# Kernel tuning notes

Measured on AMD Instinct MI355X. Metric: run time of the kernel, lower is better.

## Reference

```python
import jax, jax.numpy as jnp
import numpy as np

NUM_HEADS = 12
FEATURE_DIM = 16
HEAD_DIM = 128
EPS = 1e-12


def taylor_map(x):
    # x: [b, h, t, d] -> [b, h, t, 1 + d + d*d] (2nd-order Taylor features of exp)
    d = x.shape[-1]
    r2 = jnp.asarray(np.sqrt(2.0), x.dtype)
    rd = jnp.asarray(np.sqrt(d), x.dtype)
    rrd = jnp.asarray(np.sqrt(np.sqrt(d)), x.dtype)
    x2 = (x[..., :, None] * x[..., None, :]).reshape(x.shape[:-1] + (d * d,)) / r2
    ones = jnp.ones(x.shape[:-1] + (1,), x.dtype)
    return jnp.concatenate([ones, x / rrd, x2 / rd], axis=-1)


def setup_inputs() -> dict:
    key = jax.random.key(0)
    ks = jax.random.split(key, 5)
    b, t, hid = 2, 2048, 1536
    scale = 0.02
    return {
        "hidden_states": jax.random.normal(ks[0], (b, t, hid), jnp.float32),
        "Wq": jax.random.normal(ks[1], (NUM_HEADS * FEATURE_DIM, hid), jnp.float32) * scale,
        "Wk": jax.random.normal(ks[2], (NUM_HEADS * FEATURE_DIM, hid), jnp.float32) * scale,
        "Wv": jax.random.normal(ks[3], (NUM_HEADS * HEAD_DIM, hid), jnp.float32) * scale,
        "Wo": jax.random.normal(ks[4], (hid, NUM_HEADS * HEAD_DIM), jnp.float32) * scale,
    }


def reference(hidden_states, Wq, Wk, Wv, Wo):
    b, t, _ = hidden_states.shape
    H, dk, dv = NUM_HEADS, FEATURE_DIM, HEAD_DIM
    # projections (torch Linear: x @ W^T), split heads -> [b, h, t, d]
    q = (hidden_states @ Wq.T).reshape(b, t, H, dk).transpose(0, 2, 1, 3)
    k = (hidden_states @ Wk.T).reshape(b, t, H, dk).transpose(0, 2, 1, 3)
    v = (hidden_states @ Wv.T).reshape(b, t, H, dv).transpose(0, 2, 1, 3)
    qf = taylor_map(q)  # [b, h, t, D], D = 1 + dk + dk^2
    kf = taylor_map(k)
    # causal kernelized attention: identical math to cumsum-of-outer-products form
    S = jnp.einsum("bhtd,bhsd->bhts", qf, kf)  # [b, h, t, t]
    mask = jnp.tril(jnp.ones((t, t), bool))
    S = jnp.where(mask, S, jnp.zeros((), S.dtype))
    num = jnp.einsum("bhts,bhse->bhte", S, v)  # [b, h, t, dv]
    den = S.sum(-1) + EPS  # [b, h, t]
    y = num / den[..., None]
    y = y.transpose(0, 2, 1, 3).reshape(b, t, H * dv)
    return y @ Wo.T
```

## Files before the change

### kernel.cpp

```cpp
#include <hip/hip_runtime.h>

#define B 2
#define T 2048
#define HID 1536
#define NH 12
#define DK 16
#define DV 128
#define BT (B * T)
#define EPS 1e-12f

typedef __attribute__((ext_vector_type(8))) short bf16x8;
typedef __attribute__((ext_vector_type(4))) float f32x4;

__device__ int g_taskctr;

__device__ __forceinline__ unsigned short f2bf(float f) {
    unsigned int u = __float_as_uint(f);
    u += 0x7FFFu + ((u >> 16) & 1u);
    return (unsigned short)(u >> 16);
}

__device__ __forceinline__ unsigned int cvt_pk_bf16(float lo, float hi) {
    unsigned int r;
    asm("v_cvt_pk_bf16_f32 %0, %1, %2" : "=v"(r) : "v"(lo), "v"(hi));
    return r;
}

__global__ __launch_bounds__(256) void cvt_all(const float* __restrict__ hs,
                                               const float* __restrict__ Wq,
                                               const float* __restrict__ Wk,
                                               const float* __restrict__ Wv,
                                               const float* __restrict__ Wo,
                                               unsigned short* __restrict__ hsb,
                                               unsigned short* __restrict__ wqk,
                                               unsigned short* __restrict__ wvb,
                                               unsigned short* __restrict__ wob) {
    int bx = blockIdx.x;
    if (bx == 0 && threadIdx.x == 0) g_taskctr = 512;
    const float* src;
    unsigned short* dst;
    if (bx < 3072)      { src = hs; dst = hsb; }
    else if (bx < 3216) { src = Wq; dst = wqk;          bx -= 3072; }
    else if (bx < 3360) { src = Wk; dst = wqk + 294912; bx -= 3216; }
    else if (bx < 4512) { src = Wv; dst = wvb;          bx -= 3360; }
    else                { src = Wo; dst = wob;          bx -= 4512; }
    const int i = (bx * 256 + threadIdx.x) * 8;
    float4 a = *(const float4*)(src + i);
    float4 b = *(const float4*)(src + i + 4);
    *(ushort4*)(dst + i)     = make_ushort4(f2bf(a.x), f2bf(a.y), f2bf(a.z), f2bf(a.w));
    *(ushort4*)(dst + i + 4) = make_ushort4(f2bf(b.x), f2bf(b.y), f2bf(b.z), f2bf(b.w));
}

__device__ __forceinline__ void gemm_tile_bf16(const unsigned short* __restrict__ A,
                                               const unsigned short* __restrict__ Bm,
                                               unsigned short* __restrict__ C,
                                               int m0, int n0, int K, int ldc,
                                               unsigned short* As, unsigned short* Bs) {
    const int tid = threadIdx.x;
    const int wave = tid >> 6, lane = tid & 63;
    const int wm = (wave & 1) * 64, wn = (wave >> 1) * 64;
    const int fr = lane & 15;
    const int fk = (lane >> 4) * 8;

    f32x4 acc[4][4];
#pragma unroll
    for (int i = 0; i < 4; ++i)
#pragma unroll
        for (int j = 0; j < 4; ++j) acc[i][j] = (f32x4)0.f;

    const int c0 = tid, c1 = tid + 256;
    const int r0 = c0 >> 2, q0 = (c0 & 3) * 8;
    const int r1 = c1 >> 2, q1 = (c1 & 3) * 8;

    for (int k0 = 0; k0 < K; k0 += 32) {
        __builtin_amdgcn_global_load_lds(
            (const __attribute__((address_space(1))) void*)(A + (size_t)(m0 + r0) * K + k0 + q0),
            (__attribute__((address_space(3))) void*)(As + c0 * 8), 16, 0, 0);
        __builtin_amdgcn_global_load_lds(
            (const __attribute__((address_space(1))) void*)(A + (size_t)(m0 + r1) * K + k0 + q1),
            (__attribute__((address_space(3))) void*)(As + c1 * 8), 16, 0, 0);
        __builtin_amdgcn_global_load_lds(
            (const __attribute__((address_space(1))) void*)(Bm + (size_t)(n0 + r0) * K + k0 + q0),
            (__attribute__((address_space(3))) void*)(Bs + c0 * 8), 16, 0, 0);
        __builtin_amdgcn_global_load_lds(
            (const __attribute__((address_space(1))) void*)(Bm + (size_t)(n0 + r1) * K + k0 + q1),
            (__attribute__((address_space(3))) void*)(Bs + c1 * 8), 16, 0, 0);
        __syncthreads();

        bf16x8 af[4], bfr[4];
#pragma unroll
        for (int mb = 0; mb < 4; ++mb)
            af[mb] = *(const bf16x8*)(As + (wm + mb * 16 + fr) * 32 + fk);
#pragma unroll
        for (int nb = 0; nb < 4; ++nb)
            bfr[nb] = *(const bf16x8*)(Bs + (wn + nb * 16 + fr) * 32 + fk);
#pragma unroll
        for (int mb = 0; mb < 4; ++mb)
#pragma unroll
            for (int nb = 0; nb < 4; ++nb)
                acc[mb][nb] = __builtin_amdgcn_mfma_f32_16x16x32_bf16(
                    af[mb], bfr[nb], acc[mb][nb], 0, 0, 0);
        __syncthreads();
    }

    const int orow = (lane >> 4) * 4;
#pragma unroll
    for (int nb = 0; nb < 4; ++nb) {
        const int col = n0 + wn + nb * 16 + fr;
#pragma unroll
        for (int mb = 0; mb < 4; ++mb) {
            const int row = m0 + wm + mb * 16 + orow;
#pragma unroll
            for (int r = 0; r < 4; ++r)
                C[(size_t)(row + r) * ldc + col] = f2bf(acc[mb][nb][r]);
        }
    }
}

__global__ __launch_bounds__(256) void proj_qkv(const unsigned short* __restrict__ hsb,
                                                const unsigned short* __restrict__ wqk,
                                                const unsigned short* __restrict__ wvb,
                                                unsigned short* __restrict__ qkb,
                                                unsigned short* __restrict__ vtg) {
    __shared__ unsigned short As[128 * 32];
    __shared__ unsigned short Bs[128 * 32];
    const int bx = blockIdx.x;
    if (bx < 96) {
        gemm_tile_bf16(hsb, wqk, qkb, (bx / 3) * 128, (bx % 3) * 128, HID, 384, As, Bs);
    } else {
        const int vid = bx - 96;
        const int grp = vid / 48, sub = vid % 48;
        const int n_t = grp * 4 + (sub & 3), m_t = sub >> 2;
        gemm_tile_bf16(wvb, hsb, vtg, m_t * 128, n_t * 128, HID, BT, As, Bs);
    }
}

__global__ __launch_bounds__(256) void proj_out(const unsigned short* __restrict__ A,
                                                const unsigned short* __restrict__ Bm,
                                                float* __restrict__ C) {
    __shared__ unsigned short As[128 * 32];
    __shared__ unsigned short Bs[128 * 32];
    const int tid = threadIdx.x;
    const int m0 = blockIdx.y * 128;
    const int n0 = blockIdx.x * 128;
    const int wave = tid >> 6, lane = tid & 63;
    const int wm = (wave & 1) * 64, wn = (wave >> 1) * 64;
    const int fr = lane & 15;
    const int fk = (lane >> 4) * 8;
    const int K = HID;

    f32x4 acc[4][4];
#pragma unroll
    for (int i = 0; i < 4; ++i)
#pragma unroll
        for (int j = 0; j < 4; ++j) acc[i][j] = (f32x4)0.f;

    const int c0 = tid, c1 = tid + 256;
    const int r0 = c0 >> 2, q0 = (c0 & 3) * 8;
    const int r1 = c1 >> 2, q1 = (c1 & 3) * 8;

    for (int k0 = 0; k0 < K; k0 += 32) {
        __builtin_amdgcn_global_load_lds(
            (const __attribute__((address_space(1))) void*)(A + (size_t)(m0 + r0) * K + k0 + q0),
            (__attribute__((address_space(3))) void*)(As + c0 * 8), 16, 0, 0);
        __builtin_amdgcn_global_load_lds(
            (const __attribute__((address_space(1))) void*)(A + (size_t)(m0 + r1) * K + k0 + q1),
            (__attribute__((address_space(3))) void*)(As + c1 * 8), 16, 0, 0);
        __builtin_amdgcn_global_load_lds(
            (const __attribute__((address_space(1))) void*)(Bm + (size_t)(n0 + r0) * K + k0 + q0),
            (__attribute__((address_space(3))) void*)(Bs + c0 * 8), 16, 0, 0);
        __builtin_amdgcn_global_load_lds(
            (const __attribute__((address_space(1))) void*)(Bm + (size_t)(n0 + r1) * K + k0 + q1),
            (__attribute__((address_space(3))) void*)(Bs + c1 * 8), 16, 0, 0);
        __syncthreads();

        bf16x8 af[4], bfr[4];
#pragma unroll
        for (int mb = 0; mb < 4; ++mb)
            af[mb] = *(const bf16x8*)(As + (wm + mb * 16 + fr) * 32 + fk);
#pragma unroll
        for (int nb = 0; nb < 4; ++nb)
            bfr[nb] = *(const bf16x8*)(Bs + (wn + nb * 16 + fr) * 32 + fk);
#pragma unroll
        for (int mb = 0; mb < 4; ++mb)
#pragma unroll
            for (int nb = 0; nb < 4; ++nb)
                acc[mb][nb] = __builtin_amdgcn_mfma_f32_16x16x32_bf16(
                    af[mb], bfr[nb], acc[mb][nb], 0, 0, 0);
        __syncthreads();
    }

    const int orow = (lane >> 4) * 4;
#pragma unroll
    for (int nb = 0; nb < 4; ++nb) {
        const int col = n0 + wn + nb * 16 + fr;
#pragma unroll
        for (int mb = 0; mb < 4; ++mb) {
            const int row = m0 + wm + mb * 16 + orow;
#pragma unroll
            for (int r = 0; r < 4; ++r)
                C[(size_t)(row + r) * HID + col] = acc[mb][nb][r];
        }
    }
}

__global__ __launch_bounds__(256) void based_attn_mfma(const unsigned short* __restrict__ qk,
                                                       const unsigned short* __restrict__ vt,
                                                       unsigned short* __restrict__ yb) {
    const int tid = threadIdx.x;
    const int wave = tid >> 6, lane = tid & 63;
    const int fr = lane & 15, quad = lane >> 4;
    const int fk = quad * 8;
    const int fkk = (quad & 1) * 8;

    __shared__ __attribute__((aligned(16))) unsigned short ss[2][64][72];
    __shared__ float den_lds[64];
    __shared__ int task_s;

    int c = blockIdx.x;

    for (;;) {
        if (c >= 768) break;
        const int r = (c < 512) ? ((c & 1) ? 767 - (c >> 1) : (c >> 1)) : (c - 256);
        const int qt = 31 - r / 24;
        const int hb = r % 24;
        const int h  = hb >> 1;
        const int bi = hb & 1;

        if (tid < 64) den_lds[tid] = 0.f;

        const bf16x8 zf = {};
        bf16x8 qf[4];
#pragma unroll
        for (int nt = 0; nt < 4; ++nt) {
            qf[nt] = zf;
            if (quad < 2)
                qf[nt] = *(const bf16x8*)&qk[(size_t)(bi * T + qt * 64 + nt * 16 + fr) * 384
                                             + h * DK + fk];
        }

        f32x4 oacc[2][4];
#pragma unroll
        for (int mt = 0; mt < 2; ++mt)
#pragma unroll
            for (int nt = 0; nt < 4; ++nt) oacc[mt][nt] = (f32x4)0.f;
        float denp[4] = {0.f, 0.f, 0.f, 0.f};

        const unsigned short* kbase = qk + (size_t)(bi * T + wave * 16 + fr) * 384
                                      + 192 + h * DK + fkk;
        const unsigned short* vbase0 = vt + (size_t)(h * DV + wave * 32 + fr) * BT + bi * T + fk;
        const unsigned short* vbase1 = vbase0 + (size_t)16 * BT;

        bf16x8 kf_n = *(const bf16x8*)kbase;
        bf16x8 vf_n[2][2];
        vf_n[0][0] = *(const bf16x8*)(vbase0);
        vf_n[0][1] = *(const bf16x8*)(vbase0 + 32);
        vf_n[1][0] = *(const bf16x8*)(vbase1);
        vf_n[1][1] = *(const bf16x8*)(vbase1 + 32);

        for (int kt = 0; kt <= qt; ++kt) {
            const int bsel = kt & 1;
            const bf16x8 kf = kf_n;
            bf16x8 vf[2][2];
            vf[0][0] = vf_n[0][0]; vf[0][1] = vf_n[0][1];
            vf[1][0] = vf_n[1][0]; vf[1][1] = vf_n[1][1];

            {
                const int ktn = (kt < qt) ? kt + 1 : qt;
                kf_n = *(const bf16x8*)(kbase + (size_t)ktn * 64 * 384);
                const int off = ktn * 64;
                vf_n[0][0] = *(const bf16x8*)(vbase0 + off);
                vf_n[0][1] = *(const bf16x8*)(vbase0 + off + 32);
                vf_n[1][0] = *(const bf16x8*)(vbase1 + off);
                vf_n[1][1] = *(const bf16x8*)(vbase1 + off + 32);
            }

            f32x4 sa[4];
#pragma unroll
            for (int nt = 0; nt < 4; ++nt)
                sa[nt] = __builtin_amdgcn_mfma_f32_16x16x32_bf16(kf, qf[nt], (f32x4)0.f, 0, 0, 0);

#pragma unroll
            for (int nt = 0; nt < 4; ++nt) {
                const int i = nt * 16 + fr;
                float sv[4];
#pragma unroll
                for (int rr = 0; rr < 4; ++rr) {
                    const float a = sa[nt][rr];
                    sv[rr] = fmaf(a, fmaf(a, 1.f / 32.f, 0.25f), 1.f);
                }
                if (kt == qt) {
#pragma unroll
                    for (int rr = 0; rr < 4; ++rr) {
                        const int j = wave * 16 + quad * 4 + rr;
                        if (j > i) sv[rr] = 0.f;
                    }
                }
                denp[nt] += (sv[0] + sv[1]) + (sv[2] + sv[3]);
                uint2 pk;
                pk.x = cvt_pk_bf16(sv[0], sv[1]);
                pk.y = cvt_pk_bf16(sv[2], sv[3]);
                *(uint2*)&ss[bsel][i][wave * 16 + quad * 4] = pk;
            }
            __syncthreads();

#pragma unroll
            for (int k2 = 0; k2 < 2; ++k2) {
                bf16x8 sf[4];
#pragma unroll
                for (int nt = 0; nt < 4; ++nt)
                    sf[nt] = *(const bf16x8*)&ss[bsel][nt * 16 + fr][k2 * 32 + fk];
#pragma unroll
                for (int mt = 0; mt < 2; ++mt)
#pragma unroll
                    for (int nt = 0; nt < 4; ++nt)
                        oacc[mt][nt] = __builtin_amdgcn_mfma_f32_16x16x32_bf16(
                            vf[mt][k2], sf[nt], oacc[mt][nt], 0, 0, 0);
            }
        }

#pragma unroll
        for (int nt = 0; nt < 4; ++nt) {
            float v = denp[nt];
            v += __shfl_xor(v, 16);
            v += __shfl_xor(v, 32);
            if (quad == 0) atomicAdd(&den_lds[nt * 16 + fr], v);
        }
        __syncthreads();

#pragma unroll
        for (int nt = 0; nt < 4; ++nt) {
            const int i = nt * 16 + fr;
            const float rd = 1.f / (den_lds[i] + EPS);
            const size_t rowbase = (size_t)(bi * T + qt * 64 + i) * (NH * DV) + h * DV;
#pragma unroll
            for (int mt = 0; mt < 2; ++mt) {
                const int cc = wave * 32 + mt * 16 + quad * 4;
                const f32x4 o = oacc[mt][nt];
                *(ushort4*)&yb[rowbase + cc] = make_ushort4(f2bf(o[0] * rd), f2bf(o[1] * rd),
                                                            f2bf(o[2] * rd), f2bf(o[3] * rd));
            }
        }

        __syncthreads();
        if (tid == 0) task_s = atomicAdd(&g_taskctr, 1);
        __syncthreads();
        c = task_s;
    }
}

extern "C" void kernel_launch(void* const* d_in, const int* in_sizes, int n_in,
                              void* d_out, int out_size, void* d_ws, size_t ws_size,
                              hipStream_t stream) {
    (void)in_sizes; (void)n_in; (void)out_size; (void)ws_size;
    const float* hs = (const float*)d_in[0];
    const float* Wq = (const float*)d_in[1];
    const float* Wk = (const float*)d_in[2];
    const float* Wv = (const float*)d_in[3];
    const float* Wo = (const float*)d_in[4];
    float* out = (float*)d_out;

    unsigned short* hsb = (unsigned short*)d_ws;
    unsigned short* wqk = hsb + (size_t)BT * HID;
    unsigned short* wvb = wqk + (size_t)384 * HID;
    unsigned short* wob = wvb + (size_t)HID * HID;
    unsigned short* qkb = wob + (size_t)HID * HID;
    unsigned short* vtg = qkb + (size_t)BT * 384;
    unsigned short* ybb = vtg + (size_t)HID * BT;

    dim3 blk(256);
    cvt_all<<<dim3(5664), blk, 0, stream>>>(hs, Wq, Wk, Wv, Wo, hsb, wqk, wvb, wob);

    proj_qkv<<<dim3(480), blk, 0, stream>>>(hsb, wqk, wvb, qkb, vtg);

    based_attn_mfma<<<dim3(512), blk, 0, stream>>>(qkb, vtg, ybb);

    proj_out<<<dim3(12, 32), blk, 0, stream>>>(ybb, wob, out);
}
```

Before: 209.7 us.

## Fuse all four kernels into one persistent kernel with grid barriers

Replaces the four separate launches (conversion, QKV projection, attention, output projection) with a single persistent kernel of 512 blocks that runs each stage in turn, separated by a software grid-wide barrier built on global atomics. The aim is to remove the launch gaps and tail idle time between kernels. The cost is spin-wait barriers and fewer blocks for the conversion stage, which now loops over its work. The barrier also relies on all 512 blocks being resident at once (launch_bounds 256,2), or it can deadlock.

```diff
diff --git a/kernel.cpp b/kernel.cpp
--- a/kernel.cpp
+++ b/kernel.cpp
@@ -13,6 +13,8 @@
 typedef __attribute__((ext_vector_type(4))) float f32x4;
 
 __device__ int g_taskctr;
+__device__ unsigned g_bar_cnt = 0;
+__device__ unsigned g_bar_gen = 0;
 
 __device__ __forceinline__ unsigned short f2bf(float f) {
     unsigned int u = __float_as_uint(f);
@@ -26,29 +28,27 @@
     return r;
 }
 
-__global__ __launch_bounds__(256) void cvt_all(const float* __restrict__ hs,
-                                               const float* __restrict__ Wq,
-                                               const float* __restrict__ Wk,
-                                               const float* __restrict__ Wv,
-                                               const float* __restrict__ Wo,
-                                               unsigned short* __restrict__ hsb,
-                                               unsigned short* __restrict__ wqk,
-                                               unsigned short* __restrict__ wvb,
-                                               unsigned short* __restrict__ wob) {
-    int bx = blockIdx.x;
-    if (bx == 0 && threadIdx.x == 0) g_taskctr = 512;
-    const float* src;
-    unsigned short* dst;
-    if (bx < 3072)      { src = hs; dst = hsb; }
-    else if (bx < 3216) { src = Wq; dst = wqk;          bx -= 3072; }
-    else if (bx < 3360) { src = Wk; dst = wqk + 294912; bx -= 3216; }
-    else if (bx < 4512) { src = Wv; dst = wvb;          bx -= 3360; }
-    else                { src = Wo; dst = wob;          bx -= 4512; }
-    const int i = (bx * 256 + threadIdx.x) * 8;
-    float4 a = *(const float4*)(src + i);
-    float4 b = *(const float4*)(src + i + 4);
-    *(ushort4*)(dst + i)     = make_ushort4(f2bf(a.x), f2bf(a.y), f2bf(a.z), f2bf(a.w));
-    *(ushort4*)(dst + i + 4) = make_ushort4(f2bf(b.x), f2bf(b.y), f2bf(b.z), f2bf(b.w));
+__device__ __forceinline__ void grid_barrier() {
+    __syncthreads();
+    if (threadIdx.x == 0) {
+        __threadfence();
+        unsigned gen = __hip_atomic_load(&g_bar_gen, __ATOMIC_RELAXED,
+                                         __HIP_MEMORY_SCOPE_AGENT);
+        unsigned n = __hip_atomic_fetch_add(&g_bar_cnt, 1u, __ATOMIC_ACQ_REL,
+                                            __HIP_MEMORY_SCOPE_AGENT);
+        if (n + 1u == gridDim.x) {
+            __hip_atomic_store(&g_bar_cnt, 0u, __ATOMIC_RELAXED,
+                               __HIP_MEMORY_SCOPE_AGENT);
+            __hip_atomic_store(&g_bar_gen, gen + 1u, __ATOMIC_RELEASE,
+                               __HIP_MEMORY_SCOPE_AGENT);
+        } else {
+            while (__hip_atomic_load(&g_bar_gen, __ATOMIC_ACQUIRE,
+                                     __HIP_MEMORY_SCOPE_AGENT) == gen)
+                __builtin_amdgcn_s_sleep(1);
+        }
+        __threadfence();
+    }
+    __syncthreads();
 }
 
 __device__ __forceinline__ void gemm_tile_bf16(const unsigned short* __restrict__ A,
@@ -117,37 +117,16 @@
     }
 }
 
-__global__ __launch_bounds__(256) void proj_qkv(const unsigned short* __restrict__ hsb,
-                                                const unsigned short* __restrict__ wqk,
-                                                const unsigned short* __restrict__ wvb,
-                                                unsigned short* __restrict__ qkb,
-                                                unsigned short* __restrict__ vtg) {
-    __shared__ unsigned short As[128 * 32];
-    __shared__ unsigned short Bs[128 * 32];
-    const int bx = blockIdx.x;
-    if (bx < 96) {
-        gemm_tile_bf16(hsb, wqk, qkb, (bx / 3) * 128, (bx % 3) * 128, HID, 384, As, Bs);
-    } else {
-        const int vid = bx - 96;
-        const int grp = vid / 48, sub = vid % 48;
-        const int n_t = grp * 4 + (sub & 3), m_t = sub >> 2;
-        gemm_tile_bf16(wvb, hsb, vtg, m_t * 128, n_t * 128, HID, BT, As, Bs);
-    }
-}
-
-__global__ __launch_bounds__(256) void proj_out(const unsigned short* __restrict__ A,
-                                                const unsigned short* __restrict__ Bm,
-                                                float* __restrict__ C) {
-    __shared__ unsigned short As[128 * 32];
-    __shared__ unsigned short Bs[128 * 32];
+__device__ __forceinline__ void gemm_tile_f32(const unsigned short* __restrict__ A,
+                                              const unsigned short* __restrict__ Bm,
+                                              float* __restrict__ C,
+                                              int m0, int n0, int K, int ldc,
+                                              unsigned short* As, unsigned short* Bs) {
     const int tid = threadIdx.x;
-    const int m0 = blockIdx.y * 128;
-    const int n0 = blockIdx.x * 128;
     const int wave = tid >> 6, lane = tid & 63;
     const int wm = (wave & 1) * 64, wn = (wave >> 1) * 64;
     const int fr = lane & 15;
     const int fk = (lane >> 4) * 8;
-    const int K = HID;
 
     f32x4 acc[4][4];
 #pragma unroll
@@ -199,153 +178,211 @@
             const int row = m0 + wm + mb * 16 + orow;
 #pragma unroll
             for (int r = 0; r < 4; ++r)
-                C[(size_t)(row + r) * HID + col] = acc[mb][nb][r];
-        }
-    }
-}
-
-__global__ __launch_bounds__(256) void based_attn_mfma(const unsigned short* __restrict__ qk,
-                                                       const unsigned short* __restrict__ vt,
-                                                       unsigned short* __restrict__ yb) {
+                C[(size_t)(row + r) * ldc + col] = acc[mb][nb][r];
+        }
+    }
+}
+
+__global__ __launch_bounds__(256, 2) void fused_all(const float* __restrict__ hs,
+                                                    const float* __restrict__ Wq,
+                                                    const float* __restrict__ Wk,
+                                                    const float* __restrict__ Wv,
+                                                    const float* __restrict__ Wo,
+                                                    unsigned short* __restrict__ hsb,
+                                                    unsigned short* __restrict__ wqk,
+                                                    unsigned short* __restrict__ wvb,
+                                                    unsigned short* __restrict__ wob,
+                                                    unsigned short* __restrict__ qkb,
+                                                    unsigned short* __restrict__ vtg,
+                                                    unsigned short* __restrict__ ybb,
+                                                    float* __restrict__ out) {
+    __shared__ __attribute__((aligned(16))) unsigned short smem[9348];
+    const int bid = blockIdx.x;
     const int tid = threadIdx.x;
-    const int wave = tid >> 6, lane = tid & 63;
-    const int fr = lane & 15, quad = lane >> 4;
-    const int fk = quad * 8;
-    const int fkk = (quad & 1) * 8;
-
-    __shared__ __attribute__((aligned(16))) unsigned short ss[2][64][72];
-    __shared__ float den_lds[64];
-    __shared__ int task_s;
-
-    int c = blockIdx.x;
-
-    for (;;) {
-        if (c >= 768) break;
-        const int r = (c < 512) ? ((c & 1) ? 767 - (c >> 1) : (c >> 1)) : (c - 256);
-        const int qt = 31 - r / 24;
-        const int hb = r % 24;
-        const int h  = hb >> 1;
-        const int bi = hb & 1;
-
-        if (tid < 64) den_lds[tid] = 0.f;
-
-        const bf16x8 zf = {};
-        bf16x8 qf[4];
-#pragma unroll
-        for (int nt = 0; nt < 4; ++nt) {
-            qf[nt] = zf;
-            if (quad < 2)
-                qf[nt] = *(const bf16x8*)&qk[(size_t)(bi * T + qt * 64 + nt * 16 + fr) * 384
-                                             + h * DK + fk];
-        }
-
-        f32x4 oacc[2][4];
-#pragma unroll
-        for (int mt = 0; mt < 2; ++mt)
-#pragma unroll
-            for (int nt = 0; nt < 4; ++nt) oacc[mt][nt] = (f32x4)0.f;
-        float denp[4] = {0.f, 0.f, 0.f, 0.f};
-
-        const unsigned short* kbase = qk + (size_t)(bi * T + wave * 16 + fr) * 384
-                                      + 192 + h * DK + fkk;
-        const unsigned short* vbase0 = vt + (size_t)(h * DV + wave * 32 + fr) * BT + bi * T + fk;
-        const unsigned short* vbase1 = vbase0 + (size_t)16 * BT;
-
-        bf16x8 kf_n = *(const bf16x8*)kbase;
-        bf16x8 vf_n[2][2];
-        vf_n[0][0] = *(const bf16x8*)(vbase0);
-        vf_n[0][1] = *(const bf16x8*)(vbase0 + 32);
-        vf_n[1][0] = *(const bf16x8*)(vbase1);
-        vf_n[1][1] = *(const bf16x8*)(vbase1 + 32);
-
-        for (int kt = 0; kt <= qt; ++kt) {
-            const int bsel = kt & 1;
-            const bf16x8 kf = kf_n;
-            bf16x8 vf[2][2];
-            vf[0][0] = vf_n[0][0]; vf[0][1] = vf_n[0][1];
-            vf[1][0] = vf_n[1][0]; vf[1][1] = vf_n[1][1];
-
-            {
-                const int ktn = (kt < qt) ? kt + 1 : qt;
-                kf_n = *(const bf16x8*)(kbase + (size_t)ktn * 64 * 384);
-                const int off = ktn * 64;
-                vf_n[0][0] = *(const bf16x8*)(vbase0 + off);
-                vf_n[0][1] = *(const bf16x8*)(vbase0 + off + 32);
-                vf_n[1][0] = *(const bf16x8*)(vbase1 + off);
-                vf_n[1][1] = *(const bf16x8*)(vbase1 + off + 32);
+
+    if (bid == 0 && tid == 0) g_taskctr = 512;
+    for (int u = bid; u < 5664; u += 512) {
+        int bx = u;
+        const float* src;
+        unsigned short* dst;
+        if (bx < 3072)      { src = hs; dst = hsb; }
+        else if (bx < 3216) { src = Wq; dst = wqk;          bx -= 3072; }
+        else if (bx < 3360) { src = Wk; dst = wqk + 294912; bx -= 3216; }
+        else if (bx < 4512) { src = Wv; dst = wvb;          bx -= 3360; }
+        else                { src = Wo; dst = wob;          bx -= 4512; }
+        const int i = (bx * 256 + tid) * 8;
+        float4 a = *(const float4*)(src + i);
+        float4 b = *(const float4*)(src + i + 4);
+        *(ushort4*)(dst + i)     = make_ushort4(f2bf(a.x), f2bf(a.y), f2bf(a.z), f2bf(a.w));
+        *(ushort4*)(dst + i + 4) = make_ushort4(f2bf(b.x), f2bf(b.y), f2bf(b.z), f2bf(b.w));
+    }
+    grid_barrier();
+
+    {
+        unsigned short* As = smem;
+        unsigned short* Bs = smem + 4096;
+        if (bid < 96) {
+            gemm_tile_bf16(hsb, wqk, qkb, (bid / 3) * 128, (bid % 3) * 128, HID, 384, As, Bs);
+        } else if (bid < 480) {
+            const int vid = bid - 96;
+            const int grp = vid / 48, sub = vid % 48;
+            const int n_t = grp * 4 + (sub & 3), m_t = sub >> 2;
+            gemm_tile_bf16(wvb, hsb, vtg, m_t * 128, n_t * 128, HID, BT, As, Bs);
+        }
+    }
+    grid_barrier();
+
+    {
+        unsigned short (*ss)[64][72] = (unsigned short (*)[64][72])smem;
+        float* den_lds = (float*)(smem + 9216);
+        int* task_s = (int*)(smem + 9344);
+
+        const int wave = tid >> 6, lane = tid & 63;
+        const int fr = lane & 15, quad = lane >> 4;
+        const int fk = quad * 8;
+        const int fkk = (quad & 1) * 8;
+
+        int c = bid;
+        for (;;) {
+            if (c >= 768) break;
+            const int r = (c < 512) ? ((c & 1) ? 767 - (c >> 1) : (c >> 1)) : (c - 256);
+            const int qt = 31 - r / 24;
+            const int hb = r % 24;
+            const int h  = hb >> 1;
+            const int bi = hb & 1;
+
+            if (tid < 64) den_lds[tid] = 0.f;
+
+            const bf16x8 zf = {};
+            bf16x8 qf[4];
+#pragma unroll
+            for (int nt = 0; nt < 4; ++nt) {
+                qf[nt] = zf;
+                if (quad < 2)
+                    qf[nt] = *(const bf16x8*)&qkb[(size_t)(bi * T + qt * 64 + nt * 16 + fr) * 384
+                                                  + h * DK + fk];
             }
 
-            f32x4 sa[4];
-#pragma unroll
-            for (int nt = 0; nt < 4; ++nt)
-                sa[nt] = __builtin_amdgcn_mfma_f32_16x16x32_bf16(kf, qf[nt], (f32x4)0.f, 0, 0, 0);
+            f32x4 oacc[2][4];
+#pragma unroll
+            for (int mt = 0; mt < 2; ++mt)
+#pragma unroll
+                for (int nt = 0; nt < 4; ++nt) oacc[mt][nt] = (f32x4)0.f;
+            float denp[4] = {0.f, 0.f, 0.f, 0.f};
+
+            const unsigned short* kbase = qkb + (size_t)(bi * T + wave * 16 + fr) * 384
+                                          + 192 + h * DK + fkk;
+            const unsigned short* vbase0 = vtg + (size_t)(h * DV + wave * 32 + fr) * BT
+                                           + bi * T + fk;
+            const unsigned short* vbase1 = vbase0 + (size_t)16 * BT;
+
+            bf16x8 kf_n = *(const bf16x8*)kbase;
+            bf16x8 vf_n[2][2];
+            vf_n[0][0] = *(const bf16x8*)(vbase0);
+            vf_n[0][1] = *(const bf16x8*)(vbase0 + 32);
+            vf_n[1][0] = *(const bf16x8*)(vbase1);
+            vf_n[1][1] = *(const bf16x8*)(vbase1 + 32);
+
+            for (int kt = 0; kt <= qt; ++kt) {
+                const int bsel = kt & 1;
+                const bf16x8 kf = kf_n;
+                bf16x8 vf[2][2];
+                vf[0][0] = vf_n[0][0]; vf[0][1] = vf_n[0][1];
+                vf[1][0] = vf_n[1][0]; vf[1][1] = vf_n[1][1];
+
+                {
+                    const int ktn = (kt < qt) ? kt + 1 : qt;
+                    kf_n = *(const bf16x8*)(kbase + (size_t)ktn * 64 * 384);
+                    const int off = ktn * 64;
+                    vf_n[0][0] = *(const bf16x8*)(vbase0 + off);
+                    vf_n[0][1] = *(const bf16x8*)(vbase0 + off + 32);
+                    vf_n[1][0] = *(const bf16x8*)(vbase1 + off);
+                    vf_n[1][1] = *(const bf16x8*)(vbase1 + off + 32);
+                }
+
+                f32x4 sa[4];
+#pragma unroll
+                for (int nt = 0; nt < 4; ++nt)
+                    sa[nt] = __builtin_amdgcn_mfma_f32_16x16x32_bf16(kf, qf[nt], (f32x4)0.f,
+                                                                     0, 0, 0);
+
+#pragma unroll
+                for (int nt = 0; nt < 4; ++nt) {
+                    const int i = nt * 16 + fr;
+                    float sv[4];
+#pragma unroll
+                    for (int rr = 0; rr < 4; ++rr) {
+                        const float a = sa[nt][rr];
+                        sv[rr] = fmaf(a, fmaf(a, 1.f / 32.f, 0.25f), 1.f);
+                    }
+                    if (kt == qt) {
+#pragma unroll
+                        for (int rr = 0; rr < 4; ++rr) {
+                            const int j = wave * 16 + quad * 4 + rr;
+                            if (j > i) sv[rr] = 0.f;
+                        }
+                    }
+                    denp[nt] += (sv[0] + sv[1]) + (sv[2] + sv[3]);
+                    uint2 pk;
+                    pk.x = cvt_pk_bf16(sv[0], sv[1]);
+                    pk.y = cvt_pk_bf16(sv[2], sv[3]);
+                    *(uint2*)&ss[bsel][i][wave * 16 + quad * 4] = pk;
+                }
+                __syncthreads();
+
+#pragma unroll
+                for (int k2 = 0; k2 < 2; ++k2) {
+                    bf16x8 sf[4];
+#pragma unroll
+                    for (int nt = 0; nt < 4; ++nt)
+                        sf[nt] = *(const bf16x8*)&ss[bsel][nt * 16 + fr][k2 * 32 + fk];
+#pragma unroll
+                    for (int mt = 0; mt < 2; ++mt)
+#pragma unroll
+                        for (int nt = 0; nt < 4; ++nt)
+                            oacc[mt][nt] = __builtin_amdgcn_mfma_f32_16x16x32_bf16(
+                                vf[mt][k2], sf[nt], oacc[mt][nt], 0, 0, 0);
+                }
+            }
+
+#pragma unroll
+            for (int nt = 0; nt < 4; ++nt) {
+                float v = denp[nt];
+                v += __shfl_xor(v, 16);
+                v += __shfl_xor(v, 32);
+                if (quad == 0) atomicAdd(&den_lds[nt * 16 + fr], v);
+            }
+            __syncthreads();
 
 #pragma unroll
             for (int nt = 0; nt < 4; ++nt) {
                 const int i = nt * 16 + fr;
-                float sv[4];
-#pragma unroll
-                for (int rr = 0; rr < 4; ++rr) {
-                    const float a = sa[nt][rr];
-                    sv[rr] = fmaf(a, fmaf(a, 1.f / 32.f, 0.25f), 1.f);
+                const float rd = 1.f / (den_lds[i] + EPS);
+                const size_t rowbase = (size_t)(bi * T + qt * 64 + i) * (NH * DV) + h * DV;
+#pragma unroll
+                for (int mt = 0; mt < 2; ++mt) {
+                    const int cc = wave * 32 + mt * 16 + quad * 4;
+                    const f32x4 o = oacc[mt][nt];
+                    *(ushort4*)&ybb[rowbase + cc] = make_ushort4(f2bf(o[0] * rd), f2bf(o[1] * rd),
+                                                                 f2bf(o[2] * rd), f2bf(o[3] * rd));
                 }
-                if (kt == qt) {
-#pragma unroll
-                    for (int rr = 0; rr < 4; ++rr) {
-                        const int j = wave * 16 + quad * 4 + rr;
-                        if (j > i) sv[rr] = 0.f;
-                    }
-                }
-                denp[nt] += (sv[0] + sv[1]) + (sv[2] + sv[3]);
-                uint2 pk;
-                pk.x = cvt_pk_bf16(sv[0], sv[1]);
-                pk.y = cvt_pk_bf16(sv[2], sv[3]);
-                *(uint2*)&ss[bsel][i][wave * 16 + quad * 4] = pk;
             }
+
             __syncthreads();
-
-#pragma unroll
-            for (int k2 = 0; k2 < 2; ++k2) {
-                bf16x8 sf[4];
-#pragma unroll
-                for (int nt = 0; nt < 4; ++nt)
-                    sf[nt] = *(const bf16x8*)&ss[bsel][nt * 16 + fr][k2 * 32 + fk];
-#pragma unroll
-                for (int mt = 0; mt < 2; ++mt)
-#pragma unroll
-                    for (int nt = 0; nt < 4; ++nt)
-                        oacc[mt][nt] = __builtin_amdgcn_mfma_f32_16x16x32_bf16(
-                            vf[mt][k2], sf[nt], oacc[mt][nt], 0, 0, 0);
-            }
-        }
-
-#pragma unroll
-        for (int nt = 0; nt < 4; ++nt) {
-            float v = denp[nt];
-            v += __shfl_xor(v, 16);
-            v += __shfl_xor(v, 32);
-            if (quad == 0) atomicAdd(&den_lds[nt * 16 + fr], v);
-        }
-        __syncthreads();
-
-#pragma unroll
-        for (int nt = 0; nt < 4; ++nt) {
-            const int i = nt * 16 + fr;
-            const float rd = 1.f / (den_lds[i] + EPS);
-            const size_t rowbase = (size_t)(bi * T + qt * 64 + i) * (NH * DV) + h * DV;
-#pragma unroll
-            for (int mt = 0; mt < 2; ++mt) {
-                const int cc = wave * 32 + mt * 16 + quad * 4;
-                const f32x4 o = oacc[mt][nt];
-                *(ushort4*)&yb[rowbase + cc] = make_ushort4(f2bf(o[0] * rd), f2bf(o[1] * rd),
-                                                            f2bf(o[2] * rd), f2bf(o[3] * rd));
-            }
-        }
-
-        __syncthreads();
-        if (tid == 0) task_s = atomicAdd(&g_taskctr, 1);
-        __syncthreads();
-        c = task_s;
+            if (tid == 0) *task_s = atomicAdd(&g_taskctr, 1);
+            __syncthreads();
+            c = *task_s;
+        }
+    }
+    grid_barrier();
+
+    {
+        unsigned short* As = smem;
+        unsigned short* Bs = smem + 4096;
+        if (bid < 384) {
+            const int m_t = bid / 12, n_t = bid % 12;
+            gemm_tile_f32(ybb, wob, out, m_t * 128, n_t * 128, HID, HID, As, Bs);
+        }
     }
 }
 
@@ -368,12 +405,7 @@
     unsigned short* vtg = qkb + (size_t)BT * 384;
     unsigned short* ybb = vtg + (size_t)HID * BT;
 
-    dim3 blk(256);
-    cvt_all<<<dim3(5664), blk, 0, stream>>>(hs, Wq, Wk, Wv, Wo, hsb, wqk, wvb, wob);
-
-    proj_qkv<<<dim3(480), blk, 0, stream>>>(hsb, wqk, wvb, qkb, vtg);
-
-    based_attn_mfma<<<dim3(512), blk, 0, stream>>>(qkb, vtg, ybb);
-
-    proj_out<<<dim3(12, 32), blk, 0, stream>>>(ybb, wob, out);
-}
+    fused_all<<<dim3(512), dim3(256), 0, stream>>>(hs, Wq, Wk, Wv, Wo,
+                                                   hsb, wqk, wvb, wob,
+                                                   qkb, vtg, ybb, out);
+}
```

Result: slower. 580.2 us (+176.7%).

## Process two key tiles per barrier in causal attention loop

Applied to the files above, without the earlier changes.

The attention inner loop now handles two 64-key tiles per iteration. It computes both score tiles into a doubled shared-memory buffer and issues a single __syncthreads before the PV MFMAs for both, which halves the barrier count and doubles the register prefetch of K/V fragments. Causal masking now uses global indices, and the odd tail is handled by clamping to qt and masking the extra tile to zero. This wastes work on the padded tile when qt is even. Launch bounds add a minimum of 2 blocks per SM, which caps register use while the prefetch register footprint grows, so spills are a risk.

```diff
diff --git a/kernel.cpp b/kernel.cpp
--- a/kernel.cpp
+++ b/kernel.cpp
@@ -204,16 +204,16 @@
     }
 }
 
-__global__ __launch_bounds__(256) void based_attn_mfma(const unsigned short* __restrict__ qk,
-                                                       const unsigned short* __restrict__ vt,
-                                                       unsigned short* __restrict__ yb) {
+__global__ __launch_bounds__(256, 2) void based_attn_mfma(const unsigned short* __restrict__ qk,
+                                                          const unsigned short* __restrict__ vt,
+                                                          unsigned short* __restrict__ yb) {
     const int tid = threadIdx.x;
     const int wave = tid >> 6, lane = tid & 63;
     const int fr = lane & 15, quad = lane >> 4;
     const int fk = quad * 8;
     const int fkk = (quad & 1) * 8;
 
-    __shared__ __attribute__((aligned(16))) unsigned short ss[2][64][72];
+    __shared__ __attribute__((aligned(16))) unsigned short ss[2][2][64][72];
     __shared__ float den_lds[64];
     __shared__ int task_s;
 
@@ -251,71 +251,101 @@
         const unsigned short* vbase0 = vt + (size_t)(h * DV + wave * 32 + fr) * BT + bi * T + fk;
         const unsigned short* vbase1 = vbase0 + (size_t)16 * BT;
 
-        bf16x8 kf_n = *(const bf16x8*)kbase;
-        bf16x8 vf_n[2][2];
-        vf_n[0][0] = *(const bf16x8*)(vbase0);
-        vf_n[0][1] = *(const bf16x8*)(vbase0 + 32);
-        vf_n[1][0] = *(const bf16x8*)(vbase1);
-        vf_n[1][1] = *(const bf16x8*)(vbase1 + 32);
-
-        for (int kt = 0; kt <= qt; ++kt) {
-            const int bsel = kt & 1;
-            const bf16x8 kf = kf_n;
-            bf16x8 vf[2][2];
-            vf[0][0] = vf_n[0][0]; vf[0][1] = vf_n[0][1];
-            vf[1][0] = vf_n[1][0]; vf[1][1] = vf_n[1][1];
+        const int npair = (qt + 2) >> 1;
+
+        bf16x8 kf_n[2];
+        bf16x8 vf_n[2][2][2];
+        {
+            const int t1 = (qt >= 1) ? 1 : 0;
+            kf_n[0] = *(const bf16x8*)kbase;
+            kf_n[1] = *(const bf16x8*)(kbase + (size_t)t1 * 64 * 384);
+            const int o1 = t1 * 64;
+            vf_n[0][0][0] = *(const bf16x8*)(vbase0);
+            vf_n[0][0][1] = *(const bf16x8*)(vbase0 + 32);
+            vf_n[0][1][0] = *(const bf16x8*)(vbase1);
+            vf_n[0][1][1] = *(const bf16x8*)(vbase1 + 32);
+            vf_n[1][0][0] = *(const bf16x8*)(vbase0 + o1);
+            vf_n[1][0][1] = *(const bf16x8*)(vbase0 + o1 + 32);
+            vf_n[1][1][0] = *(const bf16x8*)(vbase1 + o1);
+            vf_n[1][1][1] = *(const bf16x8*)(vbase1 + o1 + 32);
+        }
+
+        for (int ip = 0; ip < npair; ++ip) {
+            const int p = ip & 1;
+            bf16x8 kf[2];
+            bf16x8 vf[2][2][2];
+            kf[0] = kf_n[0]; kf[1] = kf_n[1];
+#pragma unroll
+            for (int s = 0; s < 2; ++s)
+#pragma unroll
+                for (int mt = 0; mt < 2; ++mt)
+#pragma unroll
+                    for (int k2 = 0; k2 < 2; ++k2) vf[s][mt][k2] = vf_n[s][mt][k2];
 
             {
-                const int ktn = (kt < qt) ? kt + 1 : qt;
-                kf_n = *(const bf16x8*)(kbase + (size_t)ktn * 64 * 384);
-                const int off = ktn * 64;
-                vf_n[0][0] = *(const bf16x8*)(vbase0 + off);
-                vf_n[0][1] = *(const bf16x8*)(vbase0 + off + 32);
-                vf_n[1][0] = *(const bf16x8*)(vbase1 + off);
-                vf_n[1][1] = *(const bf16x8*)(vbase1 + off + 32);
+                int n0 = 2 * ip + 2; if (n0 > qt) n0 = qt;
+                int n1 = 2 * ip + 3; if (n1 > qt) n1 = qt;
+                kf_n[0] = *(const bf16x8*)(kbase + (size_t)n0 * 64 * 384);
+                kf_n[1] = *(const bf16x8*)(kbase + (size_t)n1 * 64 * 384);
+                const int o0 = n0 * 64, o1 = n1 * 64;
+                vf_n[0][0][0] = *(const bf16x8*)(vbase0 + o0);
+                vf_n[0][0][1] = *(const bf16x8*)(vbase0 + o0 + 32);
+                vf_n[0][1][0] = *(const bf16x8*)(vbase1 + o0);
+                vf_n[0][1][1] = *(const bf16x8*)(vbase1 + o0 + 32);
+                vf_n[1][0][0] = *(const bf16x8*)(vbase0 + o1);
+                vf_n[1][0][1] = *(const bf16x8*)(vbase0 + o1 + 32);
+                vf_n[1][1][0] = *(const bf16x8*)(vbase1 + o1);
+                vf_n[1][1][1] = *(const bf16x8*)(vbase1 + o1 + 32);
             }
 
-            f32x4 sa[4];
-#pragma unroll
-            for (int nt = 0; nt < 4; ++nt)
-                sa[nt] = __builtin_amdgcn_mfma_f32_16x16x32_bf16(kf, qf[nt], (f32x4)0.f, 0, 0, 0);
-
-#pragma unroll
-            for (int nt = 0; nt < 4; ++nt) {
-                const int i = nt * 16 + fr;
-                float sv[4];
-#pragma unroll
-                for (int rr = 0; rr < 4; ++rr) {
-                    const float a = sa[nt][rr];
-                    sv[rr] = fmaf(a, fmaf(a, 1.f / 32.f, 0.25f), 1.f);
+#pragma unroll
+            for (int s = 0; s < 2; ++s) {
+                const int kt = 2 * ip + s;
+                f32x4 sa[4];
+#pragma unroll
+                for (int nt = 0; nt < 4; ++nt)
+                    sa[nt] = __builtin_amdgcn_mfma_f32_16x16x32_bf16(kf[s], qf[nt],
+                                                                     (f32x4)0.f, 0, 0, 0);
+#pragma unroll
+                for (int nt = 0; nt < 4; ++nt) {
+                    const int i = nt * 16 + fr;
+                    float sv[4];
+#pragma unroll
+                    for (int rr = 0; rr < 4; ++rr) {
+                        const float a = sa[nt][rr];
+                        sv[rr] = fmaf(a, fmaf(a, 1.f / 32.f, 0.25f), 1.f);
+                    }
+                    if (kt >= qt) {
+#pragma unroll
+                        for (int rr = 0; rr < 4; ++rr) {
+                            const int jg = kt * 64 + wave * 16 + quad * 4 + rr;
+                            if (jg > qt * 64 + i) sv[rr] = 0.f;
+                        }
+                    }
+                    denp[nt] += (sv[0] + sv[1]) + (sv[2] + sv[3]);
+                    uint2 pk;
+                    pk.x = cvt_pk_bf16(sv[0], sv[1]);
+                    pk.y = cvt_pk_bf16(sv[2], sv[3]);
+                    *(uint2*)&ss[s][p][i][wave * 16 + quad * 4] = pk;
                 }
-                if (kt == qt) {
-#pragma unroll
-                    for (int rr = 0; rr < 4; ++rr) {
-                        const int j = wave * 16 + quad * 4 + rr;
-                        if (j > i) sv[rr] = 0.f;
-                    }
-                }
-                denp[nt] += (sv[0] + sv[1]) + (sv[2] + sv[3]);
-                uint2 pk;
-                pk.x = cvt_pk_bf16(sv[0], sv[1]);
-                pk.y = cvt_pk_bf16(sv[2], sv[3]);
-                *(uint2*)&ss[bsel][i][wave * 16 + quad * 4] = pk;
             }
             __syncthreads();
 
 #pragma unroll
-            for (int k2 = 0; k2 < 2; ++k2) {
-                bf16x8 sf[4];
-#pragma unroll
-                for (int nt = 0; nt < 4; ++nt)
-                    sf[nt] = *(const bf16x8*)&ss[bsel][nt * 16 + fr][k2 * 32 + fk];
-#pragma unroll
-                for (int mt = 0; mt < 2; ++mt)
+            for (int s = 0; s < 2; ++s) {
+#pragma unroll
+                for (int k2 = 0; k2 < 2; ++k2) {
+                    bf16x8 sf[4];
 #pragma unroll
                     for (int nt = 0; nt < 4; ++nt)
-                        oacc[mt][nt] = __builtin_amdgcn_mfma_f32_16x16x32_bf16(
-                            vf[mt][k2], sf[nt], oacc[mt][nt], 0, 0, 0);
+                        sf[nt] = *(const bf16x8*)&ss[s][p][nt * 16 + fr][k2 * 32 + fk];
+#pragma unroll
+                    for (int mt = 0; mt < 2; ++mt)
+#pragma unroll
+                        for (int nt = 0; nt < 4; ++nt)
+                            oacc[mt][nt] = __builtin_amdgcn_mfma_f32_16x16x32_bf16(
+                                vf[s][mt][k2], sf[nt], oacc[mt][nt], 0, 0, 0);
+                }
             }
         }
 
```

Result: no change. 211.4 us (+0.8%).
